# Performance work log

Hardware: AMD Instinct MI355X
Metric: run time of the kernel (lower is better)

The kernel has to match this reference:

```python
import jax, jax.numpy as jnp
import numpy as np

B, T, D = 4, 256, 768
NG_PER = 4          # gaussians per embedding token
OUT_DIM = 3         # color channels
EPS = 1e-6
CHUNK = 64          # gaussians processed per scan step (avoids B*N*H*W tensor)


def setup_inputs() -> dict:
    key = jax.random.key(0)
    k1, k2, k3 = jax.random.split(key, 3)
    feature = jax.random.normal(k1, (B, T, D), jnp.float32)
    # proj weight init: normal(0, 0.01)
    proj_w = jax.random.normal(k2, (NG_PER * (6 + OUT_DIM), D), jnp.float32) * 0.01
    # bias init: randn*0.01, positions slots = 0, log_scale slots = -4
    bias = jax.random.normal(k3, (NG_PER, 6 + OUT_DIM), jnp.float32) * 0.01
    bias = bias.at[:, :2].set(0.0).at[:, 2:4].set(-4.0)
    proj_b = bias.reshape(-1)
    return {"feature": feature, "proj_w": proj_w, "proj_b": proj_b, "H": 256, "W": 256}


def _splat(positions, i00, i01, i11, alphas, colors, xg, yg):
    # positions [B,N,2], i** [B,N], alphas [B,N], colors [B,N,C], xg/yg [H,W]
    Bn, N = alphas.shape
    nck = N // CHUNK

    def resh(a):  # [B,N,...] -> [nck, B, CHUNK, ...]
        return jnp.moveaxis(a.reshape(Bn, nck, CHUNK, *a.shape[2:]), 1, 0)

    xs = tuple(map(resh, (positions, i00, i01, i11, alphas, colors)))
    Hh, Ww = xg.shape
    res0 = jnp.zeros((Bn, colors.shape[-1], Hh, Ww), positions.dtype)
    ws0 = jnp.zeros((Bn, Hh, Ww), positions.dtype)

    def body(carry, chunk):
        res, ws = carry
        pos, a00, a01, a11, al, col = chunk
        dx = xg[None, None] - pos[..., 0][:, :, None, None]   # [B,CHUNK,H,W]
        dy = yg[None, None] - pos[..., 1][:, :, None, None]
        q = (a00[:, :, None, None] * dx * dx
             + 2.0 * a01[:, :, None, None] * dx * dy
             + a11[:, :, None, None] * dy * dy)
        w = jnp.exp(-0.5 * q) * al[:, :, None, None]
        res = res + jnp.einsum('bnhw,bnc->bchw', w, col)
        ws = ws + w.sum(axis=1)
        return (res, ws), None

    (res, ws), _ = jax.lax.scan(body, (res0, ws0), xs)
    return res / (ws + EPS)[:, None, :, :]


def reference(feature, proj_w, proj_b, H, W):
    # projection to per-gaussian params: [B,T,n*(6+C)] -> [B, T*n, 6+C]
    gs = feature @ proj_w.T + proj_b
    gs = gs.reshape(B, T * NG_PER, 6 + OUT_DIM)
    positions = gs[..., :2]
    log_scales = gs[..., 2:4]
    rot = gs[..., 4]
    alphas = jax.nn.sigmoid(gs[..., 5])
    colors = gs[..., 6:]
    scales = jnp.exp(log_scales)

    # covariance = R S S^T R^T + eps*I, inverted analytically (2x2)
    cos, sin = jnp.cos(rot), jnp.sin(rot)
    sx2 = scales[..., 0] ** 2
    sy2 = scales[..., 1] ** 2
    c00 = cos * cos * sx2 + sin * sin * sy2 + EPS
    c01 = cos * sin * (sx2 - sy2)
    c11 = sin * sin * sx2 + cos * cos * sy2 + EPS
    det = c00 * c11 - c01 * c01
    i00 = c11 / det
    i01 = -c01 / det
    i11 = c00 / det

    # xy grid honoring aspect ratio (xy_grid staticmethod)
    ar = H / W
    hr = ar ** 0.5
    wr = 1.0 / hr
    xg = jnp.broadcast_to(jnp.linspace(-wr, wr, W, dtype=jnp.float32)[None, :], (H, W))
    yg = jnp.broadcast_to(jnp.linspace(-hr, hr, H, dtype=jnp.float32)[:, None], (H, W))

    return _splat(positions, i00, i01, i11, alphas, colors, xg, yg)
```

## Files before the change

### kernel.cpp

```cpp
#include <hip/hip_runtime.h>
#include <math.h>

#define HH 256
#define WW 256
#define NB 4
#define NG 1024
#define DD 768
#define TH_CULL 42.0f
#define TPB 256
#define CH 128

#if __has_builtin(__builtin_amdgcn_exp2f)
#define EXP2(x) __builtin_amdgcn_exp2f(x)
#else
#define EXP2(x) exp2f(x)
#endif


__global__ __launch_bounds__(256) void param_kernel(
    const float* __restrict__ feature, const float* __restrict__ proj_w,
    const float* __restrict__ proj_b, float* __restrict__ params)
{
    __shared__ float frow[DD];
    __shared__ float gsv[36];
    const int bt  = blockIdx.x;
    const int tid = threadIdx.x;

    if (tid < DD / 4) {
        ((float4*)frow)[tid] = ((const float4*)(feature + bt * DD))[tid];
    }
    __syncthreads();

    const int wave = tid >> 6, lane = tid & 63;
    for (int i = 0; i < 9; ++i) {
        const int k = wave * 9 + i;
        const float* wrow = proj_w + k * DD;
        float s = 0.f;
        #pragma unroll
        for (int j = 0; j < DD / 64; ++j)
            s = fmaf(frow[lane + j * 64], wrow[lane + j * 64], s);
        #pragma unroll
        for (int off = 32; off; off >>= 1) s += __shfl_xor(s, off, 64);
        if (lane == 0) gsv[k] = s + proj_b[k];
    }
    __syncthreads();

    if (tid < 4) {
        const float* g = gsv + tid * 9;
        const float px = g[0], py = g[1];
        const float sx = expf(g[2]), sy = expf(g[3]);
        const float sx2 = sx * sx, sy2 = sy * sy;
        const float cs = cosf(g[4]), sn = sinf(g[4]);
        const float c00 = cs * cs * sx2 + sn * sn * sy2 + 1e-6f;
        const float c01 = cs * sn * (sx2 - sy2);
        const float c11 = sn * sn * sx2 + cs * cs * sy2 + 1e-6f;
        const float det = c00 * c11 - c01 * c01;
        const float i00 = c11 / det, i01 = -c01 / det, i11 = c00 / det;
        const float F = 0.72134752044448170368f;
        const float e00 = -F * i00;
        const float e01 = -2.f * F * i01;
        const float e11 = -F * i11;
        const float la = -log2f(1.f + expf(-g[5]));
        float* o = params + (bt * 4 + tid) * 12;
        o[0] = px;  o[1] = py;  o[2] = e00; o[3] = e01;
        o[4] = e11; o[5] = la;  o[6] = g[6]; o[7] = g[7];
        o[8] = g[8];
        o[9] = sqrtf(-(e00 + e11));
        o[10] = 0.f; o[11] = 0.f;
    }
}

__global__ __launch_bounds__(TPB) void splat_kernel(
    const float* __restrict__ params, float* __restrict__ out)
{
    __shared__ int   slist[NG];
    __shared__ float sp[CH * 12];
    __shared__ float red[48][64];
    __shared__ int   scount;

    const int blk  = blockIdx.x;
    const int tlin = blk >> 2;
    const int b    = blk & 3;
    const int tl   = (int)(__brev((unsigned)tlin) >> 24);
    const int ty   = tl >> 4, tx = tl & 15;
    const int tid  = threadIdx.x;
    const int lane = tid & 63;
    const int w4   = tid >> 6;

    if (tid == 0) scount = 0;
    __syncthreads();

    const float s2 = 2.f / 255.f;
    const float cx = -1.f + s2 * ((float)(tx * 16) + 7.5f);
    const float cy = -1.f + s2 * ((float)(ty * 16) + 7.5f);
    const float rt = s2 * 7.5f * 1.41421356f;

    const float* gp = params + b * NG * 12;

    for (int k = 0; k < 4; ++k) {
        const int gi = k * TPB + tid;
        const float4 p0 = *(const float4*)(gp + gi * 12);
        const float4 p1 = *(const float4*)(gp + gi * 12 + 4);
        const float rsq = gp[gi * 12 + 9];
        const float dx = cx - p0.x, dy = cy - p0.y;
        const float qd = -(p0.z * dx * dx + p0.w * dx * dy + p1.x * dy * dy);
        const float m  = sqrtf(fmaxf(qd, 0.f));
        const float u  = m - rt * rsq;
        const bool keep = (u <= 0.f) || (u * u <= TH_CULL + p1.y);
        const unsigned long long mask = __ballot(keep);
        int base = 0;
        if (lane == 0 && mask) base = atomicAdd(&scount, (int)__popcll(mask));
        base = __shfl(base, 0, 64);
        if (keep) {
            const int off = (int)__popcll(mask & ((1ull << lane) - 1ull));
            slist[base + off] = gi;
        }
    }
    __syncthreads();
    const int cnt = scount;

    const int xl = lane & 7, yl = lane >> 3;
    const int X0 = tx * 16 + xl, Y0 = ty * 16 + yl;
    const float xg0 = -1.f + s2 * (float)X0;
    const float xg1 = -1.f + s2 * (float)(X0 + 8);
    const float yg0 = -1.f + s2 * (float)Y0;
    const float yg1 = -1.f + s2 * (float)(Y0 + 8);

    float a00=0.f,a01=0.f,a02=0.f,a03=0.f;
    float a10=0.f,a11=0.f,a12=0.f,a13=0.f;
    float a20=0.f,a21=0.f,a22=0.f,a23=0.f;
    float a30=0.f,a31=0.f,a32=0.f,a33=0.f;

    const int nch = (cnt + CH - 1) / CH;
    for (int c = 0; c < nch; ++c) {
        const int cb = c * CH;
        const int n  = min(CH, cnt - cb);
        __syncthreads();
        for (int i = tid; i < n * 3; i += TPB) {
            const int gl = i / 3;
            const int wd = i - gl * 3;
            const int gi = slist[cb + gl];
            *(float4*)(sp + gl * 12 + wd * 4) =
                *(const float4*)(gp + gi * 12 + wd * 4);
        }
        __syncthreads();

        #pragma unroll 2
        for (int j = w4; j < n; j += 4) {
            const float* p = sp + j * 12;
            const float4 P0 = *(const float4*)p;
            const float4 P1 = *(const float4*)(p + 4);
            const float  c2 = p[8];

            const float dx0 = xg0 - P0.x, dx1 = xg1 - P0.x;
            const float ax0 = P0.z * dx0, ax1 = P0.z * dx1;
            const float dy0 = yg0 - P0.y, dy1 = yg1 - P0.y;
            const float kd0 = P0.w * dy0, kd1 = P0.w * dy1;
            const float t20 = fmaf(P1.x * dy0, dy0, P1.y);
            const float t21 = fmaf(P1.x * dy1, dy1, P1.y);

            #define PXACC(R0,R1,R2,WS,DX,AX,KD,T2) { \
                const float q = fmaf(DX, (AX) + (KD), T2); \
                const float w = EXP2(q); \
                WS += w; \
                R0 = fmaf(w, P1.z, R0); \
                R1 = fmaf(w, P1.w, R1); \
                R2 = fmaf(w, c2,  R2); }
            PXACC(a00,a01,a02,a03, dx0,ax0,kd0,t20)
            PXACC(a10,a11,a12,a13, dx1,ax1,kd0,t20)
            PXACC(a20,a21,a22,a23, dx0,ax0,kd1,t21)
            PXACC(a30,a31,a32,a33, dx1,ax1,kd1,t21)
            #undef PXACC
        }
    }

    __syncthreads();
    if (w4 > 0) {
        const int rb = (w4 - 1) * 16;
        red[rb +  0][lane] = a00; red[rb +  1][lane] = a01;
        red[rb +  2][lane] = a02; red[rb +  3][lane] = a03;
        red[rb +  4][lane] = a10; red[rb +  5][lane] = a11;
        red[rb +  6][lane] = a12; red[rb +  7][lane] = a13;
        red[rb +  8][lane] = a20; red[rb +  9][lane] = a21;
        red[rb + 10][lane] = a22; red[rb + 11][lane] = a23;
        red[rb + 12][lane] = a30; red[rb + 13][lane] = a31;
        red[rb + 14][lane] = a32; red[rb + 15][lane] = a33;
    }
    __syncthreads();
    if (w4 == 0) {
        #pragma unroll
        for (int s = 0; s < 3; ++s) {
            const int rb = s * 16;
            a00 += red[rb +  0][lane]; a01 += red[rb +  1][lane];
            a02 += red[rb +  2][lane]; a03 += red[rb +  3][lane];
            a10 += red[rb +  4][lane]; a11 += red[rb +  5][lane];
            a12 += red[rb +  6][lane]; a13 += red[rb +  7][lane];
            a20 += red[rb +  8][lane]; a21 += red[rb +  9][lane];
            a22 += red[rb + 10][lane]; a23 += red[rb + 11][lane];
            a30 += red[rb + 12][lane]; a31 += red[rb + 13][lane];
            a32 += red[rb + 14][lane]; a33 += red[rb + 15][lane];
        }
        const float i0 = 1.f / (a03 + 1e-6f);
        const float i1 = 1.f / (a13 + 1e-6f);
        const float i2 = 1.f / (a23 + 1e-6f);
        const float i3 = 1.f / (a33 + 1e-6f);

        float* ob = out + (b * 3) * (HH * WW) + Y0 * WW + X0;
        ob[0]               = a00 * i0;
        ob[HH * WW]         = a01 * i0;
        ob[2 * HH * WW]     = a02 * i0;
        ob[8]               = a10 * i1;
        ob[HH * WW + 8]     = a11 * i1;
        ob[2 * HH * WW + 8] = a12 * i1;
        ob[8 * WW]               = a20 * i2;
        ob[HH * WW + 8 * WW]     = a21 * i2;
        ob[2 * HH * WW + 8 * WW] = a22 * i2;
        ob[8 * WW + 8]               = a30 * i3;
        ob[HH * WW + 8 * WW + 8]     = a31 * i3;
        ob[2 * HH * WW + 8 * WW + 8] = a32 * i3;
    }
}

extern "C" void kernel_launch(void* const* d_in, const int* in_sizes, int n_in,
                              void* d_out, int out_size, void* d_ws, size_t ws_size,
                              hipStream_t stream) {
    const float* feature = (const float*)d_in[0];
    const float* proj_w  = (const float*)d_in[1];
    const float* proj_b  = (const float*)d_in[2];
    float* params = (float*)d_ws;
    float* out    = (float*)d_out;

    param_kernel<<<NB * 256, 256, 0, stream>>>(feature, proj_w, proj_b, params);
    splat_kernel<<<NB * 256, TPB, 0, stream>>>(params, out);
}
```

Before: 95.11 us.

## Split culling into its own kernel and parallelize splatting over four gaussian quarters

```diff
diff --git a/kernel.cpp b/kernel.cpp
--- a/kernel.cpp
+++ b/kernel.cpp
@@ -7,14 +7,14 @@
 #define NG 1024
 #define DD 768
 #define TH_CULL 42.0f
-#define TPB 256
-#define CH 128
+#define CH 64
 
 #if __has_builtin(__builtin_amdgcn_exp2f)
 #define EXP2(x) __builtin_amdgcn_exp2f(x)
 #else
 #define EXP2(x) exp2f(x)
 #endif
+
 
 
 __global__ __launch_bounds__(256) void param_kernel(
@@ -70,22 +70,17 @@
     }
 }
 
-__global__ __launch_bounds__(TPB) void splat_kernel(
-    const float* __restrict__ params, float* __restrict__ out)
-{
-    __shared__ int   slist[NG];
-    __shared__ float sp[CH * 12];
-    __shared__ float red[48][64];
-    __shared__ int   scount;
-
-    const int blk  = blockIdx.x;
-    const int tlin = blk >> 2;
-    const int b    = blk & 3;
-    const int tl   = (int)(__brev((unsigned)tlin) >> 24);
-    const int ty   = tl >> 4, tx = tl & 15;
-    const int tid  = threadIdx.x;
+__global__ __launch_bounds__(256) void cull_kernel(
+    const float* __restrict__ params, int* __restrict__ gcnt,
+    int* __restrict__ glist)
+{
+    __shared__ int scount;
+    const int blk = blockIdx.x;
+    const int b   = blk >> 8;
+    const int tl  = blk & 255;
+    const int ty  = tl >> 4, tx = tl & 15;
+    const int tid = threadIdx.x;
     const int lane = tid & 63;
-    const int w4   = tid >> 6;
 
     if (tid == 0) scount = 0;
     __syncthreads();
@@ -96,9 +91,10 @@
     const float rt = s2 * 7.5f * 1.41421356f;
 
     const float* gp = params + b * NG * 12;
+    int* lst = glist + blk * NG;
 
     for (int k = 0; k < 4; ++k) {
-        const int gi = k * TPB + tid;
+        const int gi = k * 256 + tid;
         const float4 p0 = *(const float4*)(gp + gi * 12);
         const float4 p1 = *(const float4*)(gp + gi * 12 + 4);
         const float rsq = gp[gi * 12 + 9];
@@ -113,12 +109,36 @@
         base = __shfl(base, 0, 64);
         if (keep) {
             const int off = (int)__popcll(mask & ((1ull << lane) - 1ull));
-            slist[base + off] = gi;
-        }
-    }
-    __syncthreads();
-    const int cnt = scount;
-
+            lst[base + off] = gi;
+        }
+    }
+    __syncthreads();
+    if (tid == 0) gcnt[blk] = scount;
+}
+
+__global__ __launch_bounds__(256) void splat_kernel(
+    const float* __restrict__ params, const int* __restrict__ gcnt,
+    const int* __restrict__ glist, float* __restrict__ accq)
+{
+    __shared__ float sp[CH * 12];
+    __shared__ float red[48][64];
+
+    const int blk  = blockIdx.x;
+    const int q    = blk & 3;
+    const int b    = (blk >> 2) & 3;
+    const int tl   = blk >> 4;
+    const int ty   = tl >> 4, tx = tl & 15;
+    const int tid  = threadIdx.x;
+    const int lane = tid & 63;
+    const int w4   = tid >> 6;
+
+    const int bt  = b * 256 + tl;
+    const int cnt = gcnt[bt];
+    const int K   = (cnt - q + 3) >> 2;
+    const int* lst = glist + bt * NG;
+    const float* gp = params + b * NG * 12;
+
+    const float s2 = 2.f / 255.f;
     const int xl = lane & 7, yl = lane >> 3;
     const int X0 = tx * 16 + xl, Y0 = ty * 16 + yl;
     const float xg0 = -1.f + s2 * (float)X0;
@@ -131,15 +151,13 @@
     float a20=0.f,a21=0.f,a22=0.f,a23=0.f;
     float a30=0.f,a31=0.f,a32=0.f,a33=0.f;
 
-    const int nch = (cnt + CH - 1) / CH;
-    for (int c = 0; c < nch; ++c) {
-        const int cb = c * CH;
-        const int n  = min(CH, cnt - cb);
+    for (int cb = 0; cb < K; cb += CH) {
+        const int n = min(CH, K - cb);
         __syncthreads();
-        for (int i = tid; i < n * 3; i += TPB) {
+        for (int i = tid; i < n * 3; i += 256) {
             const int gl = i / 3;
             const int wd = i - gl * 3;
-            const int gi = slist[cb + gl];
+            const int gi = lst[(cb + gl) * 4 + q];
             *(float4*)(sp + gl * 12 + wd * 4) =
                 *(const float4*)(gp + gi * 12 + wd * 4);
         }
@@ -160,8 +178,8 @@
             const float t21 = fmaf(P1.x * dy1, dy1, P1.y);
 
             #define PXACC(R0,R1,R2,WS,DX,AX,KD,T2) { \
-                const float q = fmaf(DX, (AX) + (KD), T2); \
-                const float w = EXP2(q); \
+                const float qq = fmaf(DX, (AX) + (KD), T2); \
+                const float w = EXP2(qq); \
                 WS += w; \
                 R0 = fmaf(w, P1.z, R0); \
                 R1 = fmaf(w, P1.w, R1); \
@@ -200,25 +218,60 @@
             a30 += red[rb + 12][lane]; a31 += red[rb + 13][lane];
             a32 += red[rb + 14][lane]; a33 += red[rb + 15][lane];
         }
-        const float i0 = 1.f / (a03 + 1e-6f);
-        const float i1 = 1.f / (a13 + 1e-6f);
-        const float i2 = 1.f / (a23 + 1e-6f);
-        const float i3 = 1.f / (a33 + 1e-6f);
-
-        float* ob = out + (b * 3) * (HH * WW) + Y0 * WW + X0;
-        ob[0]               = a00 * i0;
-        ob[HH * WW]         = a01 * i0;
-        ob[2 * HH * WW]     = a02 * i0;
-        ob[8]               = a10 * i1;
-        ob[HH * WW + 8]     = a11 * i1;
-        ob[2 * HH * WW + 8] = a12 * i1;
-        ob[8 * WW]               = a20 * i2;
-        ob[HH * WW + 8 * WW]     = a21 * i2;
-        ob[2 * HH * WW + 8 * WW] = a22 * i2;
-        ob[8 * WW + 8]               = a30 * i3;
-        ob[HH * WW + 8 * WW + 8]     = a31 * i3;
-        ob[2 * HH * WW + 8 * WW + 8] = a32 * i3;
-    }
+        float* ap = accq + (size_t)((q * 4 + b) * 4) * (HH * WW)
+                        + Y0 * WW + X0;
+        const int PL = HH * WW;
+        ap[0]                = a00; ap[8]                = a10;
+        ap[8 * WW]           = a20; ap[8 * WW + 8]       = a30;
+        ap[PL]               = a01; ap[PL + 8]           = a11;
+        ap[PL + 8 * WW]      = a21; ap[PL + 8 * WW + 8]  = a31;
+        ap[2*PL]             = a02; ap[2*PL + 8]         = a12;
+        ap[2*PL + 8 * WW]    = a22; ap[2*PL + 8 * WW + 8]= a32;
+        ap[3*PL]             = a03; ap[3*PL + 8]         = a13;
+        ap[3*PL + 8 * WW]    = a23; ap[3*PL + 8 * WW + 8]= a33;
+    }
+}
+
+__global__ __launch_bounds__(256) void normalize_kernel(
+    const float* __restrict__ accq, float* __restrict__ out)
+{
+    const int blk = blockIdx.x;
+    const int b   = blk >> 6, seg = blk & 63;
+    const int px  = seg * 1024 + threadIdx.x * 4;
+    const int PL  = HH * WW;
+
+    float4 r0, r1, r2, ws;
+    {
+        const float* base = accq + (size_t)((0 * 4 + b) * 4) * PL + px;
+        r0 = *(const float4*)(base);
+        r1 = *(const float4*)(base + PL);
+        r2 = *(const float4*)(base + 2 * PL);
+        ws = *(const float4*)(base + 3 * PL);
+    }
+    #pragma unroll
+    for (int q = 1; q < 4; ++q) {
+        const float* base = accq + (size_t)((q * 4 + b) * 4) * PL + px;
+        const float4 t0 = *(const float4*)(base);
+        const float4 t1 = *(const float4*)(base + PL);
+        const float4 t2 = *(const float4*)(base + 2 * PL);
+        const float4 t3 = *(const float4*)(base + 3 * PL);
+        r0.x += t0.x; r0.y += t0.y; r0.z += t0.z; r0.w += t0.w;
+        r1.x += t1.x; r1.y += t1.y; r1.z += t1.z; r1.w += t1.w;
+        r2.x += t2.x; r2.y += t2.y; r2.z += t2.z; r2.w += t2.w;
+        ws.x += t3.x; ws.y += t3.y; ws.z += t3.z; ws.w += t3.w;
+    }
+    float4 inv;
+    inv.x = 1.f / (ws.x + 1e-6f); inv.y = 1.f / (ws.y + 1e-6f);
+    inv.z = 1.f / (ws.z + 1e-6f); inv.w = 1.f / (ws.w + 1e-6f);
+
+    float* ob = out + (size_t)(b * 3) * PL + px;
+    float4 o0, o1, o2;
+    o0.x = r0.x * inv.x; o0.y = r0.y * inv.y; o0.z = r0.z * inv.z; o0.w = r0.w * inv.w;
+    o1.x = r1.x * inv.x; o1.y = r1.y * inv.y; o1.z = r1.z * inv.z; o1.w = r1.w * inv.w;
+    o2.x = r2.x * inv.x; o2.y = r2.y * inv.y; o2.z = r2.z * inv.z; o2.w = r2.w * inv.w;
+    *(float4*)(ob)          = o0;
+    *(float4*)(ob + PL)     = o1;
+    *(float4*)(ob + 2 * PL) = o2;
 }
 
 extern "C" void kernel_launch(void* const* d_in, const int* in_sizes, int n_in,
@@ -227,9 +280,16 @@
     const float* feature = (const float*)d_in[0];
     const float* proj_w  = (const float*)d_in[1];
     const float* proj_b  = (const float*)d_in[2];
+    float* out    = (float*)d_out;
+
     float* params = (float*)d_ws;
-    float* out    = (float*)d_out;
-
+    int*   gcnt   = (int*)((char*)d_ws + (4u << 20));
+    int*   glist  = (int*)((char*)d_ws + (8u << 20));
+    float* accq   = (float*)((char*)d_ws + (16u << 20));
+
+    hipMemsetAsync(accq, 0, 16u << 20, stream);
     param_kernel<<<NB * 256, 256, 0, stream>>>(feature, proj_w, proj_b, params);
-    splat_kernel<<<NB * 256, TPB, 0, stream>>>(params, out);
-}
+    cull_kernel<<<NB * 256, 256, 0, stream>>>(params, gcnt, glist);
+    splat_kernel<<<NB * 256 * 4, 256, 0, stream>>>(params, gcnt, glist, accq);
+    normalize_kernel<<<256, 256, 0, stream>>>(accq, out);
+}
```

Result: no change. 94.41 us (-0.7%).
